# Optimization experiments

Measured on AMD Instinct MI355X. Metric: run time of the kernel, lower is better.

Reference implementation:

```python
import jax, jax.numpy as jnp
import numpy as np

B, D, L = 512, 512, 24

def setup_inputs() -> dict:
    key = jax.random.key(0)
    k1, k2 = jax.random.split(key)
    source = jax.random.normal(k1, (B, D), dtype=jnp.float32)
    s_labels = jax.random.randint(k2, (B, L), 0, 2, dtype=jnp.int32)
    return {"source": source, "s_labels": s_labels}

def reference(source, s_labels):
    margin = 0.0
    squared = False
    # pairwise squared euclidean distances, (B, B)
    diff = source[:, None, :] - source[None, :, :]          # (B, B, D)
    dist = jnp.clip(jnp.sum(diff * diff, axis=-1), 0.0)     # (B, B)
    if not squared:
        zmask = (dist == 0.0).astype(dist.dtype)
        dist = jnp.sqrt(dist + zmask * 1e-16) * (1.0 - zmask)
    # triplet validity mask: labels[i]==labels[j] (share a label) and labels[i]!=labels[k]
    lab = s_labels.astype(jnp.float32)
    sim = (lab @ lab.T > 0).astype(jnp.float32)              # (B, B)
    mask = sim[:, :, None] * (1.0 - sim[:, None, :])         # (B, B, B)
    # euclidean branch: d_ap - (1 - margin) * d_an
    triplet = dist[:, :, None] - (1.0 - margin) * dist[:, None, :]
    triplet = jnp.clip(mask * triplet, 0.0)                  # (B, B, B)
    num_positive = jnp.sum((triplet > 1e-16).astype(jnp.float32))
    return jnp.sum(triplet) / (num_positive + 1e-16)
```

## Files before the change

### kernel.cpp

```cpp
#include <hip/hip_runtime.h>
#include <hip/hip_bf16.h>

#define BN 512
#define DD 512
#define LL 24

typedef unsigned short u16;
typedef __attribute__((ext_vector_type(8))) short short8;
typedef __attribute__((ext_vector_type(4))) float f32x4;


__device__ __forceinline__ float dist_val(float d2, bool diag) {
    d2 = fmaxf(d2, 0.0f);
    float d = sqrtf(d2);
    return diag ? 0.0f : d;
}

__device__ __forceinline__ unsigned pk_bf16(float lo, float hi) {
    __hip_bfloat162 p = __float22bfloat162_rn(make_float2(lo, hi));
    unsigned u;
    __builtin_memcpy(&u, &p, 4);
    return u;
}

__device__ __forceinline__ short8 pack8_pk(float4 x, float4 y, float& nrm) {
    nrm = fmaf(x.x, x.x, nrm); nrm = fmaf(x.y, x.y, nrm);
    nrm = fmaf(x.z, x.z, nrm); nrm = fmaf(x.w, x.w, nrm);
    nrm = fmaf(y.x, y.x, nrm); nrm = fmaf(y.y, y.y, nrm);
    nrm = fmaf(y.z, y.z, nrm); nrm = fmaf(y.w, y.w, nrm);
    union { uint4 u; short8 s; } cv;
    cv.u.x = pk_bf16(x.x, x.y);
    cv.u.y = pk_bf16(x.z, x.w);
    cv.u.z = pk_bf16(y.x, y.y);
    cv.u.w = pk_bf16(y.z, y.w);
    return cv.s;
}

__global__ __launch_bounds__(64) void dist_fused_kernel(
    const float* __restrict__ S, const int* __restrict__ labels,
    unsigned* __restrict__ masks, float* __restrict__ Dm, float* __restrict__ accum)
{
    const int l    = threadIdx.x;
    const int r    = l & 15;
    const int half = l >> 4;
    const int jb = blockIdx.x * 16;
    const int ib = blockIdx.y * 16;
    const int kb = half * 8;

    if (blockIdx.y == 0) {
        if (l < 16) {
            const int row = blockIdx.x * 16 + l;
            const int* lab = labels + row * LL;
            unsigned m = 0;
#pragma unroll
            for (int q = 0; q < LL; q++) m |= (lab[q] != 0 ? 1u : 0u) << q;
            masks[row] = m;
        }
        if (blockIdx.x == 0 && l == 0) { accum[0] = 0.0f; ((unsigned*)accum)[1] = 0u; }
    }

    const float* pA = S + (size_t)(ib + r) * DD + kb;
    const float* pB = S + (size_t)(jb + r) * DD + kb;

    f32x4 acc = {0.f, 0.f, 0.f, 0.f};
    float nA = 0.f, nB = 0.f;

    float4 ax = *(const float4*)pA, ay = *(const float4*)(pA + 4);
    float4 bx = *(const float4*)pB, by = *(const float4*)(pB + 4);

    for (int k0 = 0; k0 < DD; k0 += 32) {
        float4 nax, nay, nbx, nby;
        const int kn = k0 + 32;
        if (kn < DD) {
            nax = *(const float4*)(pA + kn); nay = *(const float4*)(pA + kn + 4);
            nbx = *(const float4*)(pB + kn); nby = *(const float4*)(pB + kn + 4);
        }
        short8 af = pack8_pk(ax, ay, nA);
        short8 bf = pack8_pk(bx, by, nB);
        acc = __builtin_amdgcn_mfma_f32_16x16x32_bf16(af, bf, acc, 0, 0, 0);
        ax = nax; ay = nay; bx = nbx; by = nby;
    }

    nA += __shfl_xor(nA, 16); nA += __shfl_xor(nA, 32);
    nB += __shfl_xor(nB, 16); nB += __shfl_xor(nB, 32);

    const int jc = jb + r;
    const float nj = nB;
#pragma unroll
    for (int p = 0; p < 4; p++) {
        const int ir = ib + half * 4 + p;
        const float ni = __shfl(nA, half * 4 + p);
        Dm[(size_t)ir * BN + jc] = dist_val(ni + nj - 2.f * acc[p], ir == jc);
    }
}

__global__ void triplet_kernel(const float* __restrict__ Dm, const unsigned* __restrict__ masks,
                               float* __restrict__ accum) {
    __shared__ float pos[BN];
    __shared__ float neg[BN];
    __shared__ int pcnt, ncnt;
    __shared__ float wsum[4];
    __shared__ unsigned wcnt[4];
    const int i = blockIdx.x;
    const int t = threadIdx.x;
    const int lane = t & 63;
    const int w = t >> 6;
    if (t == 0) { pcnt = 0; ncnt = 0; }
    __syncthreads();
    const unsigned mi = masks[i];
    const float* drow = Dm + (size_t)i * BN;
    const unsigned long long ltmask = (1ull << lane) - 1ull;

    for (int j = t; j < BN; j += 256) {
        float dj = drow[j];
        bool isp = (mi & masks[j]) != 0u;
        unsigned long long bal = __ballot(isp);
        int np = __popcll(bal);
        if (np > 0) {
            int ldr = __ffsll((unsigned long long)bal) - 1;
            int base = 0;
            if (lane == ldr) base = atomicAdd(&pcnt, np);
            base = __shfl(base, ldr);
            if (isp) pos[base + __popcll(bal & ltmask)] = dj;
        }
        unsigned long long nbal = ~bal;
        int nn = 64 - np;
        if (nn > 0) {
            int ldr = __ffsll((unsigned long long)nbal) - 1;
            int base = 0;
            if (lane == ldr) base = atomicAdd(&ncnt, nn);
            base = __shfl(base, ldr);
            if (!isp) neg[base + __popcll(nbal & ltmask)] = dj;
        }
    }
    __syncthreads();

    const int P = pcnt, N = ncnt;
    float sum = 0.f;
    unsigned cnt = 0;
    for (int p = t; p < P; p += 256) {
        float a = pos[p];
        for (int n = 0; n < N; n++) {
            float v = a - neg[n];
            sum += fmaxf(v, 0.0f);
            cnt += (v > 1e-16f) ? 1u : 0u;
        }
    }
#pragma unroll
    for (int off = 32; off > 0; off >>= 1) {
        sum += __shfl_down(sum, off);
        cnt += __shfl_down(cnt, off);
    }
    if (lane == 0) { wsum[w] = sum; wcnt[w] = cnt; }
    __syncthreads();
    if (t == 0) {
        sum = wsum[0] + wsum[1] + wsum[2] + wsum[3];
        cnt = wcnt[0] + wcnt[1] + wcnt[2] + wcnt[3];
        if (sum != 0.f || cnt != 0u) {
            atomicAdd(&accum[0], sum);
            atomicAdd(&((unsigned*)accum)[1], cnt);
        }
    }
}

__global__ void finalize_kernel(const float* __restrict__ accum, float* __restrict__ out) {
    if (threadIdx.x == 0) {
        float s = accum[0];
        float c = (float)((const unsigned*)accum)[1];
        out[0] = s / (c + 1e-16f);
    }
}

extern "C" void kernel_launch(void* const* d_in, const int* in_sizes, int n_in,
                              void* d_out, int out_size, void* d_ws, size_t ws_size,
                              hipStream_t stream) {
    const float* src    = (const float*)d_in[0];
    const int*   labels = (const int*)d_in[1];
    float* ws = (float*)d_ws;
    unsigned* masks = (unsigned*)ws;
    float*    Dm    = ws + BN;
    float*    accum = ws + BN + (size_t)BN * BN;

    hipLaunchKernelGGL(dist_fused_kernel, dim3(32, 32), dim3(64),  0, stream,
                       src, labels, masks, Dm, accum);
    hipLaunchKernelGGL(triplet_kernel,    dim3(BN),     dim3(256), 0, stream,
                       Dm, masks, accum);
    hipLaunchKernelGGL(finalize_kernel,   dim3(1),      dim3(64),  0, stream,
                       accum, (float*)d_out);
}
```

Baseline: 69.71 us.

## Fuse distance GEMM and triplet reduction into one block-per-16-rows kernel

Merges the distance kernel and the triplet kernel into a single kernel. Each of 32 blocks of 1024 threads computes a 16x512 stripe of distances into LDS, rebuilds all label masks locally, and then runs the pos/neg pair loop out of registers using ballots and shuffles. Per-block partial sums go to slots that a small finalize kernel reduces, replacing the global atomics. This removes the global distance matrix round trip and one launch. The cost is only 32 blocks on a large GPU, every block recomputing all label masks, and a serial loop over negatives within each wave.

```diff
diff --git a/kernel.cpp b/kernel.cpp
--- a/kernel.cpp
+++ b/kernel.cpp
@@ -4,8 +4,8 @@
 #define BN 512
 #define DD 512
 #define LL 24
+#define DSTR 516
 
-typedef unsigned short u16;
 typedef __attribute__((ext_vector_type(8))) short short8;
 typedef __attribute__((ext_vector_type(4))) float f32x4;
 
@@ -36,114 +36,106 @@
     return cv.s;
 }
 
-__global__ __launch_bounds__(64) void dist_fused_kernel(
+__global__ __launch_bounds__(1024) void fused_kernel(
     const float* __restrict__ S, const int* __restrict__ labels,
-    unsigned* __restrict__ masks, float* __restrict__ Dm, float* __restrict__ accum)
+    float* __restrict__ slots)
 {
-    const int l    = threadIdx.x;
-    const int r    = l & 15;
-    const int half = l >> 4;
-    const int jb = blockIdx.x * 16;
-    const int ib = blockIdx.y * 16;
-    const int kb = half * 8;
+    __shared__ unsigned mlds[BN];
+    __shared__ float    Dp[16 * DSTR];
+    __shared__ float    wsum[16];
+    __shared__ unsigned wcnt[16];
 
-    if (blockIdx.y == 0) {
-        if (l < 16) {
-            const int row = blockIdx.x * 16 + l;
-            const int* lab = labels + row * LL;
-            unsigned m = 0;
+    const int t    = threadIdx.x;
+    const int lane = t & 63;
+    const int w    = t >> 6;
+    const int ib   = blockIdx.x * 16;
+
+    if (t < BN) {
+        const int4* lab4 = (const int4*)(labels + (size_t)t * LL);
+        unsigned m = 0;
 #pragma unroll
-            for (int q = 0; q < LL; q++) m |= (lab[q] != 0 ? 1u : 0u) << q;
-            masks[row] = m;
+        for (int v = 0; v < 6; v++) {
+            int4 x = lab4[v];
+            m |= (x.x ? 1u : 0u) << (4 * v)
+               | (x.y ? 1u : 0u) << (4 * v + 1)
+               | (x.z ? 1u : 0u) << (4 * v + 2)
+               | (x.w ? 1u : 0u) << (4 * v + 3);
         }
-        if (blockIdx.x == 0 && l == 0) { accum[0] = 0.0f; ((unsigned*)accum)[1] = 0u; }
+        mlds[t] = m;
     }
 
-    const float* pA = S + (size_t)(ib + r) * DD + kb;
-    const float* pB = S + (size_t)(jb + r) * DD + kb;
+    const int r    = lane & 15;
+    const int half = lane >> 4;
+    const int kb   = half * 8;
+    const int j0   = w * 16;
+    const int j1   = (w + 16) * 16;
 
-    f32x4 acc = {0.f, 0.f, 0.f, 0.f};
-    float nA = 0.f, nB = 0.f;
+    const float* pA  = S + (size_t)(ib + r) * DD + kb;
+    const float* pB0 = S + (size_t)(j0 + r) * DD + kb;
+    const float* pB1 = S + (size_t)(j1 + r) * DD + kb;
 
-    float4 ax = *(const float4*)pA, ay = *(const float4*)(pA + 4);
-    float4 bx = *(const float4*)pB, by = *(const float4*)(pB + 4);
+    f32x4 acc0 = {0.f, 0.f, 0.f, 0.f}, acc1 = {0.f, 0.f, 0.f, 0.f};
+    float nA = 0.f, nB0 = 0.f, nB1 = 0.f;
+
+    float4 ax  = *(const float4*)pA,        ay  = *(const float4*)(pA + 4);
+    float4 b0x = *(const float4*)pB0,       b0y = *(const float4*)(pB0 + 4);
+    float4 b1x = *(const float4*)pB1,       b1y = *(const float4*)(pB1 + 4);
 
     for (int k0 = 0; k0 < DD; k0 += 32) {
-        float4 nax, nay, nbx, nby;
         const int kn = k0 + 32;
+        float4 nax = ax, nay = ay, nb0x = b0x, nb0y = b0y, nb1x = b1x, nb1y = b1y;
         if (kn < DD) {
-            nax = *(const float4*)(pA + kn); nay = *(const float4*)(pA + kn + 4);
-            nbx = *(const float4*)(pB + kn); nby = *(const float4*)(pB + kn + 4);
+            nax  = *(const float4*)(pA + kn);  nay  = *(const float4*)(pA + kn + 4);
+            nb0x = *(const float4*)(pB0 + kn); nb0y = *(const float4*)(pB0 + kn + 4);
+            nb1x = *(const float4*)(pB1 + kn); nb1y = *(const float4*)(pB1 + kn + 4);
         }
-        short8 af = pack8_pk(ax, ay, nA);
-        short8 bf = pack8_pk(bx, by, nB);
-        acc = __builtin_amdgcn_mfma_f32_16x16x32_bf16(af, bf, acc, 0, 0, 0);
-        ax = nax; ay = nay; bx = nbx; by = nby;
+        short8 af  = pack8_pk(ax,  ay,  nA);
+        short8 bf0 = pack8_pk(b0x, b0y, nB0);
+        short8 bf1 = pack8_pk(b1x, b1y, nB1);
+        acc0 = __builtin_amdgcn_mfma_f32_16x16x32_bf16(af, bf0, acc0, 0, 0, 0);
+        acc1 = __builtin_amdgcn_mfma_f32_16x16x32_bf16(af, bf1, acc1, 0, 0, 0);
+        ax = nax; ay = nay; b0x = nb0x; b0y = nb0y; b1x = nb1x; b1y = nb1y;
     }
 
-    nA += __shfl_xor(nA, 16); nA += __shfl_xor(nA, 32);
-    nB += __shfl_xor(nB, 16); nB += __shfl_xor(nB, 32);
+    nA  += __shfl_xor(nA, 16);  nA  += __shfl_xor(nA, 32);
+    nB0 += __shfl_xor(nB0, 16); nB0 += __shfl_xor(nB0, 32);
+    nB1 += __shfl_xor(nB1, 16); nB1 += __shfl_xor(nB1, 32);
 
-    const int jc = jb + r;
-    const float nj = nB;
 #pragma unroll
     for (int p = 0; p < 4; p++) {
-        const int ir = ib + half * 4 + p;
-        const float ni = __shfl(nA, half * 4 + p);
-        Dm[(size_t)ir * BN + jc] = dist_val(ni + nj - 2.f * acc[p], ir == jc);
+        const int il = half * 4 + p;
+        const int gi = ib + il;
+        const float ni = __shfl(nA, il);
+        Dp[il * DSTR + j0 + r] = dist_val(ni + nB0 - 2.f * acc0[p], gi == (j0 + r));
+        Dp[il * DSTR + j1 + r] = dist_val(ni + nB1 - 2.f * acc1[p], gi == (j1 + r));
     }
-}
 
-__global__ void triplet_kernel(const float* __restrict__ Dm, const unsigned* __restrict__ masks,
-                               float* __restrict__ accum) {
-    __shared__ float pos[BN];
-    __shared__ float neg[BN];
-    __shared__ int pcnt, ncnt;
-    __shared__ float wsum[4];
-    __shared__ unsigned wcnt[4];
-    const int i = blockIdx.x;
-    const int t = threadIdx.x;
-    const int lane = t & 63;
-    const int w = t >> 6;
-    if (t == 0) { pcnt = 0; ncnt = 0; }
-    __syncthreads();
-    const unsigned mi = masks[i];
-    const float* drow = Dm + (size_t)i * BN;
-    const unsigned long long ltmask = (1ull << lane) - 1ull;
-
-    for (int j = t; j < BN; j += 256) {
-        float dj = drow[j];
-        bool isp = (mi & masks[j]) != 0u;
-        unsigned long long bal = __ballot(isp);
-        int np = __popcll(bal);
-        if (np > 0) {
-            int ldr = __ffsll((unsigned long long)bal) - 1;
-            int base = 0;
-            if (lane == ldr) base = atomicAdd(&pcnt, np);
-            base = __shfl(base, ldr);
-            if (isp) pos[base + __popcll(bal & ltmask)] = dj;
-        }
-        unsigned long long nbal = ~bal;
-        int nn = 64 - np;
-        if (nn > 0) {
-            int ldr = __ffsll((unsigned long long)nbal) - 1;
-            int base = 0;
-            if (lane == ldr) base = atomicAdd(&ncnt, nn);
-            base = __shfl(base, ldr);
-            if (!isp) neg[base + __popcll(nbal & ltmask)] = dj;
-        }
-    }
     __syncthreads();
 
-    const int P = pcnt, N = ncnt;
-    float sum = 0.f;
-    unsigned cnt = 0;
-    for (int p = t; p < P; p += 256) {
-        float a = pos[p];
-        for (int n = 0; n < N; n++) {
-            float v = a - neg[n];
-            sum += fmaxf(v, 0.0f);
-            cnt += (v > 1e-16f) ? 1u : 0u;
+    const unsigned mi = mlds[ib + w];
+    float dv[8]; unsigned long long pb[8];
+#pragma unroll
+    for (int c = 0; c < 8; c++) {
+        const int j = c * 64 + lane;
+        dv[c] = Dp[w * DSTR + j];
+        pb[c] = __ballot((mi & mlds[j]) != 0u);
+    }
+    float sum = 0.f; unsigned cnt = 0;
+#pragma unroll
+    for (int c = 0; c < 8; c++) {
+        unsigned long long nb = ~pb[c];
+        while (nb) {
+            const int k = __ffsll(nb) - 1;
+            nb &= nb - 1;
+            const float dk = __shfl(dv[c], k);
+#pragma unroll
+            for (int c2 = 0; c2 < 8; c2++) {
+                if ((pb[c2] >> lane) & 1ull) {
+                    const float v = dv[c2] - dk;
+                    sum += fmaxf(v, 0.0f);
+                    cnt += (v > 1e-16f) ? 1u : 0u;
+                }
+            }
         }
     }
 #pragma unroll
@@ -153,22 +145,29 @@
     }
     if (lane == 0) { wsum[w] = sum; wcnt[w] = cnt; }
     __syncthreads();
+
     if (t == 0) {
-        sum = wsum[0] + wsum[1] + wsum[2] + wsum[3];
-        cnt = wcnt[0] + wcnt[1] + wcnt[2] + wcnt[3];
-        if (sum != 0.f || cnt != 0u) {
-            atomicAdd(&accum[0], sum);
-            atomicAdd(&((unsigned*)accum)[1], cnt);
-        }
+        float s = 0.f; unsigned c = 0;
+#pragma unroll
+        for (int q = 0; q < 16; q++) { s += wsum[q]; c += wcnt[q]; }
+        slots[blockIdx.x * 2]                   = s;
+        ((unsigned*)slots)[blockIdx.x * 2 + 1]  = c;
     }
 }
 
-__global__ void finalize_kernel(const float* __restrict__ accum, float* __restrict__ out) {
-    if (threadIdx.x == 0) {
-        float s = accum[0];
-        float c = (float)((const unsigned*)accum)[1];
-        out[0] = s / (c + 1e-16f);
+__global__ void finalize_kernel(const float* __restrict__ slots, float* __restrict__ out) {
+    const int t = threadIdx.x;
+    float s = 0.f; unsigned c = 0;
+    if (t < 32) {
+        s = slots[t * 2];
+        c = ((const unsigned*)slots)[t * 2 + 1];
     }
+#pragma unroll
+    for (int off = 32; off > 0; off >>= 1) {
+        s += __shfl_down(s, off);
+        c += __shfl_down(c, off);
+    }
+    if (t == 0) out[0] = s / ((float)c + 1e-16f);
 }
 
 extern "C" void kernel_launch(void* const* d_in, const int* in_sizes, int n_in,
@@ -176,15 +175,8 @@
                               hipStream_t stream) {
     const float* src    = (const float*)d_in[0];
     const int*   labels = (const int*)d_in[1];
-    float* ws = (float*)d_ws;
-    unsigned* masks = (unsigned*)ws;
-    float*    Dm    = ws + BN;
-    float*    accum = ws + BN + (size_t)BN * BN;
+    float* slots = (float*)d_ws;
 
-    hipLaunchKernelGGL(dist_fused_kernel, dim3(32, 32), dim3(64),  0, stream,
-                       src, labels, masks, Dm, accum);
-    hipLaunchKernelGGL(triplet_kernel,    dim3(BN),     dim3(256), 0, stream,
-                       Dm, masks, accum);
-    hipLaunchKernelGGL(finalize_kernel,   dim3(1),      dim3(64),  0, stream,
-                       accum, (float*)d_out);
+    hipLaunchKernelGGL(fused_kernel,    dim3(32), dim3(1024), 0, stream, src, labels, slots);
+    hipLaunchKernelGGL(finalize_kernel, dim3(1),  dim3(64),   0, stream, slots, (float*)d_out);
 }
```

Measured after the change: 104.1 us. +49.4%, slower.

## Rewrite triplet stage with wave ballots and fold finalize into last block

Applied to the files above, without the earlier changes.

Replaces the 512-block LDS-compaction triplet kernel with 128 single-wave blocks that each handle 4 anchor rows. Positive/negative membership is kept as ballot bitmasks and negatives are broadcast with shuffles. Rows with no negatives are skipped before their distance row is loaded. The separate finalize kernel is removed: a global completion counter lets the last block compute the output, which saves a launch but adds fences and atomics.

```diff
diff --git a/kernel.cpp b/kernel.cpp
--- a/kernel.cpp
+++ b/kernel.cpp
@@ -5,7 +5,6 @@
 #define DD 512
 #define LL 24
 
-typedef unsigned short u16;
 typedef __attribute__((ext_vector_type(8))) short short8;
 typedef __attribute__((ext_vector_type(4))) float f32x4;
 
@@ -56,7 +55,11 @@
             for (int q = 0; q < LL; q++) m |= (lab[q] != 0 ? 1u : 0u) << q;
             masks[row] = m;
         }
-        if (blockIdx.x == 0 && l == 0) { accum[0] = 0.0f; ((unsigned*)accum)[1] = 0u; }
+        if (blockIdx.x == 0 && l == 0) {
+            accum[0] = 0.0f;
+            ((unsigned*)accum)[1] = 0u;
+            ((unsigned*)accum)[2] = 0u;
+        }
     }
 
     const float* pA = S + (size_t)(ib + r) * DD + kb;
@@ -94,80 +97,77 @@
     }
 }
 
-__global__ void triplet_kernel(const float* __restrict__ Dm, const unsigned* __restrict__ masks,
-                               float* __restrict__ accum) {
-    __shared__ float pos[BN];
-    __shared__ float neg[BN];
-    __shared__ int pcnt, ncnt;
-    __shared__ float wsum[4];
-    __shared__ unsigned wcnt[4];
-    const int i = blockIdx.x;
-    const int t = threadIdx.x;
-    const int lane = t & 63;
-    const int w = t >> 6;
-    if (t == 0) { pcnt = 0; ncnt = 0; }
-    __syncthreads();
-    const unsigned mi = masks[i];
-    const float* drow = Dm + (size_t)i * BN;
-    const unsigned long long ltmask = (1ull << lane) - 1ull;
+#define K2_BLOCKS 128
+#define K2_ROWS   (BN / K2_BLOCKS)
 
-    for (int j = t; j < BN; j += 256) {
-        float dj = drow[j];
-        bool isp = (mi & masks[j]) != 0u;
-        unsigned long long bal = __ballot(isp);
-        int np = __popcll(bal);
-        if (np > 0) {
-            int ldr = __ffsll((unsigned long long)bal) - 1;
-            int base = 0;
-            if (lane == ldr) base = atomicAdd(&pcnt, np);
-            base = __shfl(base, ldr);
-            if (isp) pos[base + __popcll(bal & ltmask)] = dj;
+__global__ __launch_bounds__(64) void triplet_kernel(
+    const float* __restrict__ Dm, const unsigned* __restrict__ masks,
+    float* __restrict__ accum, float* __restrict__ out)
+{
+    const int lane = threadIdx.x;
+
+    unsigned m[8];
+#pragma unroll
+    for (int c = 0; c < 8; c++) m[c] = masks[c * 64 + lane];
+
+    float bsum = 0.f; unsigned bcnt = 0;
+
+    for (int rr = 0; rr < K2_ROWS; rr++) {
+        const int i = blockIdx.x * K2_ROWS + rr;
+        const unsigned mi = masks[i];
+
+        unsigned long long pb[8];
+        unsigned long long anyneg = 0ull;
+#pragma unroll
+        for (int c = 0; c < 8; c++) {
+            pb[c] = __ballot((mi & m[c]) != 0u);
+            anyneg |= ~pb[c];
         }
-        unsigned long long nbal = ~bal;
-        int nn = 64 - np;
-        if (nn > 0) {
-            int ldr = __ffsll((unsigned long long)nbal) - 1;
-            int base = 0;
-            if (lane == ldr) base = atomicAdd(&ncnt, nn);
-            base = __shfl(base, ldr);
-            if (!isp) neg[base + __popcll(nbal & ltmask)] = dj;
+        if (anyneg == 0ull) continue;
+
+        const float* drow = Dm + (size_t)i * BN;
+        float dv[8];
+#pragma unroll
+        for (int c = 0; c < 8; c++) dv[c] = drow[c * 64 + lane];
+
+#pragma unroll
+        for (int c = 0; c < 8; c++) {
+            unsigned long long nb = ~pb[c];
+            while (nb) {
+                const int k = __ffsll(nb) - 1;
+                nb &= nb - 1;
+                const float dk = __shfl(dv[c], k);
+#pragma unroll
+                for (int c2 = 0; c2 < 8; c2++) {
+                    if ((pb[c2] >> lane) & 1ull) {
+                        const float v = dv[c2] - dk;
+                        bsum += fmaxf(v, 0.0f);
+                        bcnt += (v > 1e-16f) ? 1u : 0u;
+                    }
+                }
+            }
         }
     }
-    __syncthreads();
 
-    const int P = pcnt, N = ncnt;
-    float sum = 0.f;
-    unsigned cnt = 0;
-    for (int p = t; p < P; p += 256) {
-        float a = pos[p];
-        for (int n = 0; n < N; n++) {
-            float v = a - neg[n];
-            sum += fmaxf(v, 0.0f);
-            cnt += (v > 1e-16f) ? 1u : 0u;
-        }
-    }
 #pragma unroll
     for (int off = 32; off > 0; off >>= 1) {
-        sum += __shfl_down(sum, off);
-        cnt += __shfl_down(cnt, off);
+        bsum += __shfl_down(bsum, off);
+        bcnt += __shfl_down(bcnt, off);
     }
-    if (lane == 0) { wsum[w] = sum; wcnt[w] = cnt; }
-    __syncthreads();
-    if (t == 0) {
-        sum = wsum[0] + wsum[1] + wsum[2] + wsum[3];
-        cnt = wcnt[0] + wcnt[1] + wcnt[2] + wcnt[3];
-        if (sum != 0.f || cnt != 0u) {
-            atomicAdd(&accum[0], sum);
-            atomicAdd(&((unsigned*)accum)[1], cnt);
+    if (lane == 0 && (bsum != 0.f || bcnt != 0u)) {
+        atomicAdd(&accum[0], bsum);
+        atomicAdd(&((unsigned*)accum)[1], bcnt);
+    }
+
+    __threadfence();
+    if (lane == 0) {
+        const unsigned t = atomicAdd(&((unsigned*)accum)[2], 1u);
+        if (t == (unsigned)(K2_BLOCKS - 1)) {
+            __threadfence();
+            const float    s = atomicAdd(&accum[0], 0.0f);
+            const unsigned c = atomicAdd(&((unsigned*)accum)[1], 0u);
+            out[0] = s / ((float)c + 1e-16f);
         }
-    }
-}
-
-__global__ void finalize_kernel(const float* __restrict__ accum, float* __restrict__ out) {
-    if (threadIdx.x == 0) {
-        float s = accum[0];
-        float c = (float)((const unsigned*)accum)[1];
-        out[0] = s / (c + 1e-16f);
     }
 }
 
@@ -181,10 +181,8 @@
     float*    Dm    = ws + BN;
     float*    accum = ws + BN + (size_t)BN * BN;
 
-    hipLaunchKernelGGL(dist_fused_kernel, dim3(32, 32), dim3(64),  0, stream,
+    hipLaunchKernelGGL(dist_fused_kernel, dim3(32, 32),   dim3(64), 0, stream,
                        src, labels, masks, Dm, accum);
-    hipLaunchKernelGGL(triplet_kernel,    dim3(BN),     dim3(256), 0, stream,
-                       Dm, masks, accum);
-    hipLaunchKernelGGL(finalize_kernel,   dim3(1),      dim3(64),  0, stream,
-                       accum, (float*)d_out);
+    hipLaunchKernelGGL(triplet_kernel,    dim3(K2_BLOCKS), dim3(64), 0, stream,
+                       Dm, masks, accum, (float*)d_out);
 }
```

New measurement: 71.43 us. +2.5%, slower.

## Split distance GEMM K-dimension across four waves with LDS reduction

Applied to the files above, without the earlier changes.

The distance kernel now launches 256 threads per 16x16 tile, and each of four waves handles a 128-wide slice of the 512-element feature dimension. Partial MFMA accumulators and row norms go into shared memory, and wave 0 sums them before writing the distance. The aim is to shorten each block's serial 16-step MFMA/load chain and expose more memory-level parallelism. In exchange it adds shared-memory traffic, a block barrier, and three idle waves during the epilogue.

```diff
diff --git a/kernel.cpp b/kernel.cpp
--- a/kernel.cpp
+++ b/kernel.cpp
@@ -36,27 +36,33 @@
     return cv.s;
 }
 
-__global__ __launch_bounds__(64) void dist_fused_kernel(
+__global__ __launch_bounds__(256) void dist_fused_kernel(
     const float* __restrict__ S, const int* __restrict__ labels,
     unsigned* __restrict__ masks, float* __restrict__ Dm, float* __restrict__ accum)
 {
-    const int l    = threadIdx.x;
-    const int r    = l & 15;
-    const int half = l >> 4;
+    __shared__ f32x4 accL[4][64];
+    __shared__ float nAL[4][16];
+    __shared__ float nBL[4][16];
+
+    const int t    = threadIdx.x;
+    const int lane = t & 63;
+    const int w    = t >> 6;
+    const int r    = lane & 15;
+    const int half = lane >> 4;
     const int jb = blockIdx.x * 16;
     const int ib = blockIdx.y * 16;
-    const int kb = half * 8;
+    const int kb = w * 128 + half * 8;
 
     if (blockIdx.y == 0) {
-        if (l < 16) {
-            const int row = blockIdx.x * 16 + l;
+        if (t < 16) {
+            const int row = blockIdx.x * 16 + t;
             const int* lab = labels + row * LL;
             unsigned m = 0;
 #pragma unroll
             for (int q = 0; q < LL; q++) m |= (lab[q] != 0 ? 1u : 0u) << q;
             masks[row] = m;
         }
-        if (blockIdx.x == 0 && l == 0) { accum[0] = 0.0f; ((unsigned*)accum)[1] = 0u; }
+        if (blockIdx.x == 0 && t == 0) { accum[0] = 0.0f; ((unsigned*)accum)[1] = 0u; }
     }
 
     const float* pA = S + (size_t)(ib + r) * DD + kb;
@@ -68,10 +74,11 @@
     float4 ax = *(const float4*)pA, ay = *(const float4*)(pA + 4);
     float4 bx = *(const float4*)pB, by = *(const float4*)(pB + 4);
 
-    for (int k0 = 0; k0 < DD; k0 += 32) {
+#pragma unroll
+    for (int k0 = 0; k0 < 128; k0 += 32) {
         float4 nax, nay, nbx, nby;
         const int kn = k0 + 32;
-        if (kn < DD) {
+        if (kn < 128) {
             nax = *(const float4*)(pA + kn); nay = *(const float4*)(pA + kn + 4);
             nbx = *(const float4*)(pB + kn); nby = *(const float4*)(pB + kn + 4);
         }
@@ -84,13 +91,23 @@
     nA += __shfl_xor(nA, 16); nA += __shfl_xor(nA, 32);
     nB += __shfl_xor(nB, 16); nB += __shfl_xor(nB, 32);
 
+    accL[w][lane] = acc;
+    if (lane < 16) { nAL[w][lane] = nA; nBL[w][lane] = nB; }
+    __syncthreads();
+    if (w != 0) return;
+
+    const f32x4 a0 = accL[0][lane], a1 = accL[1][lane],
+                a2 = accL[2][lane], a3 = accL[3][lane];
+    f32x4 accT = a0 + a1 + a2 + a3;
+    const float njt = nBL[0][r] + nBL[1][r] + nBL[2][r] + nBL[3][r];
+
     const int jc = jb + r;
-    const float nj = nB;
 #pragma unroll
     for (int p = 0; p < 4; p++) {
-        const int ir = ib + half * 4 + p;
-        const float ni = __shfl(nA, half * 4 + p);
-        Dm[(size_t)ir * BN + jc] = dist_val(ni + nj - 2.f * acc[p], ir == jc);
+        const int il = half * 4 + p;
+        const int ir = ib + il;
+        const float ni = nAL[0][il] + nAL[1][il] + nAL[2][il] + nAL[3][il];
+        Dm[(size_t)ir * BN + jc] = dist_val(ni + njt - 2.f * accT[p], ir == jc);
     }
 }
 
@@ -181,7 +198,7 @@
     float*    Dm    = ws + BN;
     float*    accum = ws + BN + (size_t)BN * BN;
 
-    hipLaunchKernelGGL(dist_fused_kernel, dim3(32, 32), dim3(64),  0, stream,
+    hipLaunchKernelGGL(dist_fused_kernel, dim3(32, 32), dim3(256), 0, stream,
                        src, labels, masks, Dm, accum);
     hipLaunchKernelGGL(triplet_kernel,    dim3(BN),     dim3(256), 0, stream,
                        Dm, masks, accum);
```

New measurement: 68.92 us (median of 2 runs). About the same (-1.1%).
